# Kernel optimization log

Measured on AMD Instinct MI355X. Metric: run time of the kernel, lower is better.

## Reference

```python
import math
import jax, jax.numpy as jnp
import numpy as np

HIDDEN = 1024
N_HEADS = 16
HEAD = HIDDEN // N_HEADS
B = 2
L = 2048
STRIDE = 128
EXPR = 8
MAXPOS = 2048


def _checkpoint(wi):
    if wi % STRIDE == 0 and wi != 0:
        return wi - EXPR
    return (wi // STRIDE) * STRIDE + STRIDE - EXPR


def _subset_summaries(absolute_max):
    ci = _checkpoint(0)
    s = set()
    while ci <= absolute_max - 1:
        s |= set(range(ci, min(ci + EXPR + 1, absolute_max)))
        ci = _checkpoint(ci + STRIDE)
    return s


def build_sparse_mask(n, bidirectional=True):
    # Faithful numpy port of prepare_sparse_mask: -1e4 everywhere, 0 at allowed positions.
    mask = np.full((n, n), -10000.0, dtype=np.float32)
    global_summaries = _subset_summaries(n) if bidirectional else set()
    for i in range(n):
        absolute_max = n if bidirectional else i + 1
        rounded = ((i + STRIDE) // STRIDE) * STRIDE
        if i % STRIDE == 0 and i != 0:
            s1 = set(range(i - STRIDE, min(absolute_max, i + 1)))
        else:
            s1 = set(range(max(0, rounded - STRIDE), min(absolute_max, rounded + 1)))
        s2 = set() if bidirectional else _subset_summaries(absolute_max)
        idx = sorted(s1 | s2 | global_summaries)
        mask[i, idx] = 0.0
    return mask


def setup_inputs() -> dict:
    key = jax.random.key(0)
    ks = jax.random.split(key, 8)
    s = 1.0 / math.sqrt(HIDDEN)
    inp = {
        "hidden_states": jax.random.normal(ks[0], (B, L, HIDDEN), dtype=jnp.float32),
        "attention_mask": jnp.zeros((B, 1, 1, L), dtype=jnp.float32),
        "Wq": jax.random.normal(ks[1], (HIDDEN, HIDDEN), dtype=jnp.float32) * s,
        "bq": jnp.zeros((HIDDEN,), dtype=jnp.float32),
        "Wk": jax.random.normal(ks[2], (HIDDEN, HIDDEN), dtype=jnp.float32) * s,
        "bk": jnp.zeros((HIDDEN,), dtype=jnp.float32),
        "Wv": jax.random.normal(ks[3], (HIDDEN, HIDDEN), dtype=jnp.float32) * s,
        "bv": jnp.zeros((HIDDEN,), dtype=jnp.float32),
        "sparse_mask": jnp.asarray(build_sparse_mask(MAXPOS)[:L, :L]),
    }
    return inp


def _split_heads(x):  # [B, L, H] -> [B, nH, L, hd]
    b, l, _ = x.shape
    return x.reshape(b, l, N_HEADS, HEAD).transpose(0, 2, 1, 3)


def reference(hidden_states, attention_mask, Wq, bq, Wk, bk, Wv, bv, sparse_mask):
    q = _split_heads(hidden_states @ Wq + bq)
    k = _split_heads(hidden_states @ Wk + bk)
    v = _split_heads(hidden_states @ Wv + bv)
    scores = jnp.einsum("bhqd,bhkd->bhqk", q, k) / math.sqrt(HEAD)
    scores = scores + sparse_mask  # [L,L] broadcasts over [B,nH,L,L]
    scores = jnp.clip(scores, -10000.0, 10000.0)
    scores = scores + attention_mask
    probs = jax.nn.softmax(scores.astype(jnp.float32), axis=-1).astype(scores.dtype)
    # dropout prob = 0.0 -> identity
    ctx = jnp.einsum("bhqk,bhkd->bhqd", probs, v)
    return ctx.transpose(0, 2, 1, 3).reshape(hidden_states.shape[0], -1, HIDDEN)
```

## Files before the change

### kernel.cpp

```cpp
#include <hip/hip_runtime.h>

#define HID 1024
#define NH 16
#define HD 64
#define BB 2
#define LL 2048
#define GC 143
#define GP 192

typedef __attribute__((ext_vector_type(8))) __bf16 bf16x8;
typedef __attribute__((ext_vector_type(4))) float f32x4;

__device__ __forceinline__ void gload_lds16(const void* g, void* l) {
  __builtin_amdgcn_global_load_lds((const __attribute__((address_space(1))) void*)g,
                                   (__attribute__((address_space(3))) void*)l, 16, 0, 0);
}

__global__ __launch_bounds__(256) void cvt_hs_kernel(const float* __restrict__ hs,
                                                     __bf16* __restrict__ hsb) {
  int i = blockIdx.x * 256 + threadIdx.x;
  const float4* src = (const float4*)hs;
  float4 a = src[2 * i], b = src[2 * i + 1];
  bf16x8 v;
  v[0] = (__bf16)a.x; v[1] = (__bf16)a.y; v[2] = (__bf16)a.z; v[3] = (__bf16)a.w;
  v[4] = (__bf16)b.x; v[5] = (__bf16)b.y; v[6] = (__bf16)b.z; v[7] = (__bf16)b.w;
  ((bf16x8*)hsb)[i] = v;
}

__global__ __launch_bounds__(256) void cvt_wt_kernel(const float* __restrict__ Wq,
                                                     const float* __restrict__ Wk,
                                                     const float* __restrict__ Wv,
                                                     __bf16* __restrict__ wtb) {
  int kt = blockIdx.x, nt = blockIdx.y, z = blockIdx.z;
  const float* w = (z == 0) ? Wq : (z == 1) ? Wk : Wv;
  __bf16* dst = wtb + (size_t)z * HID * HID;
  __shared__ __bf16 tile[64][66];
  int t = threadIdx.x;
  int cr = t & 63, rr = t >> 6;
#pragma unroll
  for (int it = 0; it < 16; it++) {
    int r = it * 4 + rr;
    tile[cr][r] = (__bf16)w[(size_t)(kt * 64 + r) * HID + nt * 64 + cr];
  }
  __syncthreads();
#pragma unroll
  for (int it = 0; it < 16; it++) {
    int r = it * 4 + rr;
    dst[(size_t)(nt * 64 + r) * HID + kt * 64 + cr] = tile[r][cr];
  }
}

__global__ __launch_bounds__(256) void setup_kernel(const float* __restrict__ amask,
                                                    unsigned int* __restrict__ zbase,
                                                    float* __restrict__ amg) {
  int i = blockIdx.x * 256 + threadIdx.x;
  zbase[i] = 0u;
  if (i < BB * GP) {
    int b = i / GP, cc = i % GP;
    int k = cc / 9, j = cc - 9 * k;
    int col = (cc < GC) ? (120 + 128 * k + j) : 0;
    amg[i] = amask[b * LL + col];
  }
}

__global__ __launch_bounds__(256, 2) void qkv_gemm_kernel(
    const __bf16* __restrict__ hsb, const __bf16* __restrict__ wtb,
    const float* __restrict__ bq, const float* __restrict__ bk,
    const float* __restrict__ bv, __bf16* __restrict__ qb,
    __bf16* __restrict__ kkb, __bf16* __restrict__ vtb,
    __bf16* __restrict__ kgb, __bf16* __restrict__ vgb) {
  int nt = blockIdx.x, mt = blockIdx.y, which = blockIdx.z;
  const __bf16* wt = wtb + (size_t)which * HID * HID;
  const float* bias = (which == 0) ? bq : (which == 1) ? bk : bv;

  __shared__ __bf16 a_lds[128 * 64];
  __shared__ __bf16 b_lds[128 * 64];

  int tid = threadIdx.x;
  int wave = tid >> 6, lane = tid & 63;
  int wm = wave >> 1, wn = wave & 1;
  int lrow = lane & 15, lgr = lane >> 4, g = lane & 7;

  f32x4 acc[4][4];
#pragma unroll
  for (int i = 0; i < 4; i++)
#pragma unroll
    for (int j = 0; j < 4; j++) acc[i][j] = f32x4{0.f, 0.f, 0.f, 0.f};

  for (int kk = 0; kk < HID; kk += 64) {
#pragma unroll
    for (int i = 0; i < 4; i++) {
      int r = (wave * 4 + i) * 8 + (lane >> 3);
      int gs = (g ^ (r & 7)) * 8;
      gload_lds16(hsb + (size_t)(mt * 128 + r) * HID + kk + gs,
                  &a_lds[(wave * 4 + i) * 512]);
      gload_lds16(wt + (size_t)(nt * 128 + r) * HID + kk + gs,
                  &b_lds[(wave * 4 + i) * 512]);
    }
    __syncthreads();
#pragma unroll
    for (int kf = 0; kf < 2; kf++) {
      bf16x8 af[4], bfr[4];
#pragma unroll
      for (int mr = 0; mr < 4; mr++) {
        int row = wm * 64 + mr * 16 + lrow;
        af[mr] = *(const bf16x8*)((const char*)a_lds + row * 128 +
                                  ((kf * 64 + lgr * 16) ^ ((row & 7) << 4)));
      }
#pragma unroll
      for (int nr = 0; nr < 4; nr++) {
        int row = wn * 64 + nr * 16 + lrow;
        bfr[nr] = *(const bf16x8*)((const char*)b_lds + row * 128 +
                                   ((kf * 64 + lgr * 16) ^ ((row & 7) << 4)));
      }
#pragma unroll
      for (int mr = 0; mr < 4; mr++)
#pragma unroll
        for (int nr = 0; nr < 4; nr++)
          acc[mr][nr] = __builtin_amdgcn_mfma_f32_16x16x32_bf16(
              af[mr], bfr[nr], acc[mr][nr], 0, 0, 0);
    }
    __syncthreads();
  }

#pragma unroll
  for (int nr = 0; nr < 4; nr++) {
    int n = nt * 128 + wn * 64 + nr * 16 + lrow;
    float bsv = bias[n];
    int hh = n >> 6, d = n & 63;
#pragma unroll
    for (int mr = 0; mr < 4; mr++) {
#pragma unroll
      for (int reg = 0; reg < 4; reg++) {
        int m = mt * 128 + wm * 64 + mr * 16 + lgr * 4 + reg;
        int bidx = m >> 11, l = m & 2047;
        float val = acc[mr][nr][reg] + bsv;
        int c7 = l & 127;
        bool isg = (c7 >= 120) || (c7 == 0 && l != 0);
        int cidx = (c7 >= 120) ? ((l >> 7) * 9 + (c7 - 120)) : (((l >> 7) - 1) * 9 + 8);
        if (which == 0) {
          val *= 0.125f;
          qb[((size_t)(bidx * NH + hh) * LL + l) * HD + d] = (__bf16)val;
        } else if (which == 1) {
          __bf16 bv16 = (__bf16)val;
          kkb[((size_t)(bidx * NH + hh) * LL + l) * HD + d] = bv16;
          if (isg) kgb[((size_t)(bidx * NH + hh) * GP + cidx) * HD + d] = bv16;
        } else {
          __bf16 bv16 = (__bf16)val;
          vtb[((size_t)(bidx * NH + hh) * HD + d) * LL + l] = bv16;
          if (isg) vgb[((size_t)(bidx * NH + hh) * HD + d) * GP + cidx] = bv16;
        }
      }
    }
  }
}

__global__ __launch_bounds__(512, 4) void attn_kernel(
    const __bf16* __restrict__ qb, const __bf16* __restrict__ kkb,
    const __bf16* __restrict__ vtb, const __bf16* __restrict__ kgb,
    const __bf16* __restrict__ vgb, const float* __restrict__ amg,
    const float* __restrict__ amask, float* __restrict__ out) {
  __shared__ __bf16 kbuf[2][64 * 64];
  __shared__ __bf16 vbuf[2][64 * 64];
  __shared__ __bf16 p_scr[8][16 * 64];

  int qt = blockIdx.x, hh = blockIdx.y, b = blockIdx.z;
  int tid = threadIdx.x, wave = tid >> 6, lane = tid & 63;
  int lrow = lane & 15, lgr = lane >> 4, g = lane & 7;

  const __bf16* qbh = qb + (size_t)(b * NH + hh) * LL * HD;
  const __bf16* kbh = kkb + (size_t)(b * NH + hh) * LL * HD;
  const __bf16* vth = vtb + (size_t)(b * NH + hh) * HD * LL;
  const __bf16* kgh = kgb + (size_t)(b * NH + hh) * GP * HD;
  const __bf16* vgh = vgb + (size_t)(b * NH + hh) * HD * GP;

  int shift = (qt == 16) ? 0 : 1;
  int qt2 = (qt == 16) ? 0 : qt;
  int W = qt2 * 128;

  int qrow = qt2 * 128 + shift + wave * 16 + lrow;
  int qld = (qrow > LL - 1) ? (LL - 1) : qrow;
  bf16x8 qf0 = *(const bf16x8*)(qbh + (size_t)qld * HD + lgr * 8);
  bf16x8 qf1 = *(const bf16x8*)(qbh + (size_t)qld * HD + 32 + lgr * 8);

  float amG[3][4], amL[2][4];
#pragma unroll
  for (int it = 0; it < 3; it++)
#pragma unroll
    for (int nr = 0; nr < 4; nr++) {
      int cc = it * 64 + nr * 16 + lrow;
      amG[it][nr] = (cc < GC) ? amg[b * GP + cc] : 0.f;
    }
#pragma unroll
  for (int it = 0; it < 2; it++)
#pragma unroll
    for (int nr = 0; nr < 4; nr++)
      amL[it][nr] = amask[b * LL + W + it * 64 + nr * 16 + lrow];

  const float M0 = 20.f;
  float l_part[4];
  f32x4 o_acc[4];
#pragma unroll
  for (int i = 0; i < 4; i++) {
    l_part[i] = 0.f;
    o_acc[i] = f32x4{0.f, 0.f, 0.f, 0.f};
  }
  int myrow = qt2 * 128 + shift + wave * 16 + lgr * 4;

#define STAGE(IT, BI)                                                     \
  do {                                                                    \
    const __bf16 *ks_, *vs_;                                              \
    int vst_;                                                             \
    if ((IT) < 3) {                                                       \
      ks_ = kgh + (size_t)((IT)*64) * HD;                                 \
      vs_ = vgh + (IT)*64;                                                \
      vst_ = GP;                                                          \
    } else {                                                              \
      int cb_ = W + ((IT)-3) * 64;                                        \
      ks_ = kbh + (size_t)cb_ * HD;                                       \
      vs_ = vth + cb_;                                                    \
      vst_ = LL;                                                          \
    }                                                                     \
    int r_ = tid >> 3;                                                    \
    int gs_ = (g ^ (r_ & 7)) * 8;                                         \
    gload_lds16(ks_ + (size_t)r_ * HD + gs_, &kbuf[BI][wave * 512]);      \
    gload_lds16(vs_ + (size_t)r_ * vst_ + gs_, &vbuf[BI][wave * 512]);    \
  } while (0)

  STAGE(0, 0);
  __syncthreads();

#pragma unroll
  for (int it = 0; it < 5; it++) {
    int cur = it & 1;
    if (it < 4) STAGE(it + 1, cur ^ 1);

    const __bf16* k_lds = kbuf[cur];
    const __bf16* v_lds = vbuf[cur];
    int colbase = (it < 3) ? it * 64 : W + (it - 3) * 64;

    f32x4 s[4];
#pragma unroll
    for (int nr = 0; nr < 4; nr++) {
      int row = nr * 16 + lrow;
      bf16x8 kf0 = *(const bf16x8*)((const char*)k_lds + row * 128 +
                                    ((lgr * 16) ^ ((row & 7) << 4)));
      bf16x8 kf1 = *(const bf16x8*)((const char*)k_lds + row * 128 +
                                    ((64 + lgr * 16) ^ ((row & 7) << 4)));
      f32x4 z = f32x4{0.f, 0.f, 0.f, 0.f};
      z = __builtin_amdgcn_mfma_f32_16x16x32_bf16(qf0, kf0, z, 0, 0, 0);
      z = __builtin_amdgcn_mfma_f32_16x16x32_bf16(qf1, kf1, z, 0, 0, 0);
      s[nr] = z;
    }

#pragma unroll
    for (int nr = 0; nr < 4; nr++) {
      if (it < 3) {
        int cc = colbase + nr * 16 + lrow;
        float am = amG[it][nr];
#pragma unroll
        for (int reg = 0; reg < 4; reg++) {
          float v = fminf(fmaxf(s[nr][reg], -10000.f), 10000.f) + am;
          if (cc >= GC) v = -10000.f;
          s[nr][reg] = v;
        }
      } else {
        int off = (it - 3) * 64 + nr * 16 + lrow;
        float am = amL[it - 3][nr];
        bool gcol = (off >= 120) || (off == 0 && W != 0);
#pragma unroll
        for (int reg = 0; reg < 4; reg++) {
          float v = s[nr][reg] + (gcol ? -10000.f : 0.f);
          v = fminf(fmaxf(v, -10000.f), 10000.f) + am;
          s[nr][reg] = v;
        }
      }
    }

#pragma unroll
    for (int reg = 0; reg < 4; reg++) {
#pragma unroll
      for (int nr = 0; nr < 4; nr++) {
        float p = __expf(s[nr][reg] - M0);
        s[nr][reg] = p;
        l_part[reg] += p;
      }
    }

#pragma unroll
    for (int nr = 0; nr < 4; nr++) {
#pragma unroll
      for (int reg = 0; reg < 4; reg++) {
        int rq = lgr * 4 + reg;
        int off = (nr * 32 + lrow * 2) ^ ((rq & 7) << 4);
        *(__bf16*)((char*)&p_scr[wave][0] + rq * 128 + off) = (__bf16)s[nr][reg];
      }
    }
    asm volatile("s_waitcnt lgkmcnt(0)" ::: "memory");
    __builtin_amdgcn_sched_barrier(0);

    bf16x8 pa0 = *(const bf16x8*)((const char*)&p_scr[wave][0] + lrow * 128 +
                                  ((lgr * 16) ^ ((lrow & 7) << 4)));
    bf16x8 pa1 = *(const bf16x8*)((const char*)&p_scr[wave][0] + lrow * 128 +
                                  ((64 + lgr * 16) ^ ((lrow & 7) << 4)));
#pragma unroll
    for (int nd = 0; nd < 4; nd++) {
      int row = nd * 16 + lrow;
      bf16x8 vf0 = *(const bf16x8*)((const char*)v_lds + row * 128 +
                                    ((lgr * 16) ^ ((row & 7) << 4)));
      bf16x8 vf1 = *(const bf16x8*)((const char*)v_lds + row * 128 +
                                    ((64 + lgr * 16) ^ ((row & 7) << 4)));
      o_acc[nd] = __builtin_amdgcn_mfma_f32_16x16x32_bf16(pa0, vf0, o_acc[nd], 0, 0, 0);
      o_acc[nd] = __builtin_amdgcn_mfma_f32_16x16x32_bf16(pa1, vf1, o_acc[nd], 0, 0, 0);
    }
    __syncthreads();
  }
#undef STAGE

#pragma unroll
  for (int off = 1; off < 16; off <<= 1)
#pragma unroll
    for (int reg = 0; reg < 4; reg++) l_part[reg] += __shfl_xor(l_part[reg], off);

#pragma unroll
  for (int nd = 0; nd < 4; nd++) {
#pragma unroll
    for (int reg = 0; reg < 4; reg++) {
      int row = myrow + reg;
      if (row < LL) {
        int d = nd * 16 + lrow;
        out[((size_t)b * LL + row) * HID + hh * HD + d] =
            o_acc[nd][reg] / l_part[reg];
      }
    }
  }
}

extern "C" void kernel_launch(void* const* d_in, const int* in_sizes, int n_in,
                              void* d_out, int out_size, void* d_ws, size_t ws_size,
                              hipStream_t stream) {
  (void)in_sizes; (void)n_in; (void)out_size; (void)ws_size;
  const float* hs = (const float*)d_in[0];
  const float* amask = (const float*)d_in[1];
  const float* Wq = (const float*)d_in[2];
  const float* bq = (const float*)d_in[3];
  const float* Wk = (const float*)d_in[4];
  const float* bk = (const float*)d_in[5];
  const float* Wv = (const float*)d_in[6];
  const float* bv = (const float*)d_in[7];
  float* out = (float*)d_out;

  char* ws = (char*)d_ws;
  __bf16* hsb = (__bf16*)(ws);
  __bf16* wtb = (__bf16*)(ws + 8388608);
  __bf16* qb  = (__bf16*)(ws + 14680064);
  __bf16* kb  = (__bf16*)(ws + 23068672);
  __bf16* vtb = (__bf16*)(ws + 31457280);
  __bf16* kgb = (__bf16*)(ws + 39845888);
  __bf16* vgb = (__bf16*)(ws + 40632320);
  float*  amg = (float*)(ws + 41418752);

  hipLaunchKernelGGL(cvt_hs_kernel, dim3(2048), dim3(256), 0, stream, hs, hsb);
  hipLaunchKernelGGL(cvt_wt_kernel, dim3(16, 16, 3), dim3(256), 0, stream, Wq, Wk, Wv, wtb);
  hipLaunchKernelGGL(setup_kernel, dim3(1536), dim3(256), 0, stream,
                     amask, (unsigned int*)kgb, amg);
  hipLaunchKernelGGL(qkv_gemm_kernel, dim3(8, 32, 3), dim3(256), 0, stream,
                     hsb, wtb, bq, bk, bv, qb, kb, vtb, kgb, vgb);
  hipLaunchKernelGGL(attn_kernel, dim3(17, NH, BB), dim3(512), 0, stream,
                     qb, kb, vtb, kgb, vgb, amg, amask, out);
}
```

Measured before the change: 75.23 us.

## Merge prep kernels into one launch and read K/V directly from global

Fuses the three preprocessing kernels (hidden-state bf16 conversion, weight transpose-convert, mask/zero setup) into one kernel that dispatches on block index, saving two launches. The attention kernel drops its double-buffered LDS staging of K and V tiles and the per-iteration barriers, loading MFMA operands straight from global memory (L2/cache). The intent is to remove launch overhead and synchronisation, at the cost of redundant global/cache traffic, since all 8 waves reread the same K/V tiles, and uncoalesced strided loads for V.

Result: slower. 102.1 us (+35.7%).

```diff
diff --git a/kernel.cpp b/kernel.cpp
--- a/kernel.cpp
+++ b/kernel.cpp
@@ -16,50 +16,49 @@
                                    (__attribute__((address_space(3))) void*)l, 16, 0, 0);
 }
 
-__global__ __launch_bounds__(256) void cvt_hs_kernel(const float* __restrict__ hs,
-                                                     __bf16* __restrict__ hsb) {
-  int i = blockIdx.x * 256 + threadIdx.x;
-  const float4* src = (const float4*)hs;
-  float4 a = src[2 * i], b = src[2 * i + 1];
-  bf16x8 v;
-  v[0] = (__bf16)a.x; v[1] = (__bf16)a.y; v[2] = (__bf16)a.z; v[3] = (__bf16)a.w;
-  v[4] = (__bf16)b.x; v[5] = (__bf16)b.y; v[6] = (__bf16)b.z; v[7] = (__bf16)b.w;
-  ((bf16x8*)hsb)[i] = v;
-}
-
-__global__ __launch_bounds__(256) void cvt_wt_kernel(const float* __restrict__ Wq,
-                                                     const float* __restrict__ Wk,
-                                                     const float* __restrict__ Wv,
-                                                     __bf16* __restrict__ wtb) {
-  int kt = blockIdx.x, nt = blockIdx.y, z = blockIdx.z;
-  const float* w = (z == 0) ? Wq : (z == 1) ? Wk : Wv;
-  __bf16* dst = wtb + (size_t)z * HID * HID;
-  __shared__ __bf16 tile[64][66];
+__global__ __launch_bounds__(256) void prep_kernel(
+    const float* __restrict__ hs, __bf16* __restrict__ hsb,
+    const float* __restrict__ Wq, const float* __restrict__ Wk,
+    const float* __restrict__ Wv, __bf16* __restrict__ wtb,
+    const float* __restrict__ amask, unsigned int* __restrict__ zbase,
+    float* __restrict__ amg) {
+  int bx = blockIdx.x;
   int t = threadIdx.x;
-  int cr = t & 63, rr = t >> 6;
-#pragma unroll
-  for (int it = 0; it < 16; it++) {
-    int r = it * 4 + rr;
-    tile[cr][r] = (__bf16)w[(size_t)(kt * 64 + r) * HID + nt * 64 + cr];
-  }
-  __syncthreads();
-#pragma unroll
-  for (int it = 0; it < 16; it++) {
-    int r = it * 4 + rr;
-    dst[(size_t)(nt * 64 + r) * HID + kt * 64 + cr] = tile[r][cr];
-  }
-}
-
-__global__ __launch_bounds__(256) void setup_kernel(const float* __restrict__ amask,
-                                                    unsigned int* __restrict__ zbase,
-                                                    float* __restrict__ amg) {
-  int i = blockIdx.x * 256 + threadIdx.x;
-  zbase[i] = 0u;
-  if (i < BB * GP) {
-    int b = i / GP, cc = i % GP;
-    int k = cc / 9, j = cc - 9 * k;
-    int col = (cc < GC) ? (120 + 128 * k + j) : 0;
-    amg[i] = amask[b * LL + col];
+  if (bx < 2048) {
+    int i = bx * 256 + t;
+    const float4* src = (const float4*)hs;
+    float4 a = src[2 * i], b = src[2 * i + 1];
+    bf16x8 v;
+    v[0] = (__bf16)a.x; v[1] = (__bf16)a.y; v[2] = (__bf16)a.z; v[3] = (__bf16)a.w;
+    v[4] = (__bf16)b.x; v[5] = (__bf16)b.y; v[6] = (__bf16)b.z; v[7] = (__bf16)b.w;
+    ((bf16x8*)hsb)[i] = v;
+  } else if (bx < 2048 + 768) {
+    int z3 = bx - 2048;
+    int kt = z3 & 15, nt = (z3 >> 4) & 15, z = z3 >> 8;
+    const float* w = (z == 0) ? Wq : (z == 1) ? Wk : Wv;
+    __bf16* dst = wtb + (size_t)z * HID * HID;
+    __shared__ __bf16 tile[64][66];
+    int cr = t & 63, rr = t >> 6;
+#pragma unroll
+    for (int it = 0; it < 16; it++) {
+      int r = it * 4 + rr;
+      tile[cr][r] = (__bf16)w[(size_t)(kt * 64 + r) * HID + nt * 64 + cr];
+    }
+    __syncthreads();
+#pragma unroll
+    for (int it = 0; it < 16; it++) {
+      int r = it * 4 + rr;
+      dst[(size_t)(nt * 64 + r) * HID + kt * 64 + cr] = tile[r][cr];
+    }
+  } else {
+    int i = (bx - 2816) * 256 + t;
+    zbase[i] = 0u;
+    if (i < BB * GP) {
+      int b = i / GP, cc = i % GP;
+      int k = cc / 9, j = cc - 9 * k;
+      int col = (cc < GC) ? (120 + 128 * k + j) : 0;
+      amg[i] = amask[b * LL + col];
+    }
   }
 }
 
@@ -160,13 +159,11 @@
     const __bf16* __restrict__ vtb, const __bf16* __restrict__ kgb,
     const __bf16* __restrict__ vgb, const float* __restrict__ amg,
     const float* __restrict__ amask, float* __restrict__ out) {
-  __shared__ __bf16 kbuf[2][64 * 64];
-  __shared__ __bf16 vbuf[2][64 * 64];
   __shared__ __bf16 p_scr[8][16 * 64];
 
   int qt = blockIdx.x, hh = blockIdx.y, b = blockIdx.z;
   int tid = threadIdx.x, wave = tid >> 6, lane = tid & 63;
-  int lrow = lane & 15, lgr = lane >> 4, g = lane & 7;
+  int lrow = lane & 15, lgr = lane >> 4;
 
   const __bf16* qbh = qb + (size_t)(b * NH + hh) * LL * HD;
   const __bf16* kbh = kkb + (size_t)(b * NH + hh) * LL * HD;
@@ -207,46 +204,28 @@
   }
   int myrow = qt2 * 128 + shift + wave * 16 + lgr * 4;
 
-#define STAGE(IT, BI)                                                     \
-  do {                                                                    \
-    const __bf16 *ks_, *vs_;                                              \
-    int vst_;                                                             \
-    if ((IT) < 3) {                                                       \
-      ks_ = kgh + (size_t)((IT)*64) * HD;                                 \
-      vs_ = vgh + (IT)*64;                                                \
-      vst_ = GP;                                                          \
-    } else {                                                              \
-      int cb_ = W + ((IT)-3) * 64;                                        \
-      ks_ = kbh + (size_t)cb_ * HD;                                       \
-      vs_ = vth + cb_;                                                    \
-      vst_ = LL;                                                          \
-    }                                                                     \
-    int r_ = tid >> 3;                                                    \
-    int gs_ = (g ^ (r_ & 7)) * 8;                                         \
-    gload_lds16(ks_ + (size_t)r_ * HD + gs_, &kbuf[BI][wave * 512]);      \
-    gload_lds16(vs_ + (size_t)r_ * vst_ + gs_, &vbuf[BI][wave * 512]);    \
-  } while (0)
-
-  STAGE(0, 0);
-  __syncthreads();
-
 #pragma unroll
   for (int it = 0; it < 5; it++) {
-    int cur = it & 1;
-    if (it < 4) STAGE(it + 1, cur ^ 1);
-
-    const __bf16* k_lds = kbuf[cur];
-    const __bf16* v_lds = vbuf[cur];
-    int colbase = (it < 3) ? it * 64 : W + (it - 3) * 64;
+    const __bf16 *ksrc, *vsrc;
+    int vstride, colbase;
+    if (it < 3) {
+      colbase = it * 64;
+      ksrc = kgh + (size_t)colbase * HD;
+      vsrc = vgh + colbase;
+      vstride = GP;
+    } else {
+      colbase = W + (it - 3) * 64;
+      ksrc = kbh + (size_t)colbase * HD;
+      vsrc = vth + colbase;
+      vstride = LL;
+    }
 
     f32x4 s[4];
 #pragma unroll
     for (int nr = 0; nr < 4; nr++) {
       int row = nr * 16 + lrow;
-      bf16x8 kf0 = *(const bf16x8*)((const char*)k_lds + row * 128 +
-                                    ((lgr * 16) ^ ((row & 7) << 4)));
-      bf16x8 kf1 = *(const bf16x8*)((const char*)k_lds + row * 128 +
-                                    ((64 + lgr * 16) ^ ((row & 7) << 4)));
+      bf16x8 kf0 = *(const bf16x8*)(ksrc + (size_t)row * HD + lgr * 8);
+      bf16x8 kf1 = *(const bf16x8*)(ksrc + (size_t)row * HD + 32 + lgr * 8);
       f32x4 z = f32x4{0.f, 0.f, 0.f, 0.f};
       z = __builtin_amdgcn_mfma_f32_16x16x32_bf16(qf0, kf0, z, 0, 0, 0);
       z = __builtin_amdgcn_mfma_f32_16x16x32_bf16(qf1, kf1, z, 0, 0, 0);
@@ -306,16 +285,12 @@
 #pragma unroll
     for (int nd = 0; nd < 4; nd++) {
       int row = nd * 16 + lrow;
-      bf16x8 vf0 = *(const bf16x8*)((const char*)v_lds + row * 128 +
-                                    ((lgr * 16) ^ ((row & 7) << 4)));
-      bf16x8 vf1 = *(const bf16x8*)((const char*)v_lds + row * 128 +
-                                    ((64 + lgr * 16) ^ ((row & 7) << 4)));
+      bf16x8 vf0 = *(const bf16x8*)(vsrc + (size_t)row * vstride + lgr * 8);
+      bf16x8 vf1 = *(const bf16x8*)(vsrc + (size_t)row * vstride + 32 + lgr * 8);
       o_acc[nd] = __builtin_amdgcn_mfma_f32_16x16x32_bf16(pa0, vf0, o_acc[nd], 0, 0, 0);
       o_acc[nd] = __builtin_amdgcn_mfma_f32_16x16x32_bf16(pa1, vf1, o_acc[nd], 0, 0, 0);
     }
-    __syncthreads();
-  }
-#undef STAGE
+  }
 
 #pragma unroll
   for (int off = 1; off < 16; off <<= 1)
@@ -360,10 +335,8 @@
   __bf16* vgb = (__bf16*)(ws + 40632320);
   float*  amg = (float*)(ws + 41418752);
 
-  hipLaunchKernelGGL(cvt_hs_kernel, dim3(2048), dim3(256), 0, stream, hs, hsb);
-  hipLaunchKernelGGL(cvt_wt_kernel, dim3(16, 16, 3), dim3(256), 0, stream, Wq, Wk, Wv, wtb);
-  hipLaunchKernelGGL(setup_kernel, dim3(1536), dim3(256), 0, stream,
-                     amask, (unsigned int*)kgb, amg);
+  hipLaunchKernelGGL(prep_kernel, dim3(4352), dim3(256), 0, stream,
+                     hs, hsb, Wq, Wk, Wv, wtb, amask, (unsigned int*)kgb, amg);
   hipLaunchKernelGGL(qkv_gemm_kernel, dim3(8, 32, 3), dim3(256), 0, stream,
                      hsb, wtb, bq, bk, bv, qb, kb, vtb, kgb, vgb);
   hipLaunchKernelGGL(attn_kernel, dim3(17, NH, BB), dim3(512), 0, stream,
```
